# Optimization experiments

Measured on AMD Instinct MI355X. Metric: run time of the kernel, lower is better.

## Reference

```python
import jax, jax.numpy as jnp
import numpy as np

LAMBDA_ORD = 1.0
B, C = 65536, 256


def setup_inputs() -> dict:
    key = jax.random.key(0)
    k1, k2 = jax.random.split(key)
    predictions = jax.random.normal(k1, (B, C), dtype=jnp.float32)
    targets = jax.random.randint(k2, (B,), 0, C, dtype=jnp.int64)
    return {"predictions": predictions, "targets": targets}


def reference(predictions, targets):
    # Cross-entropy with mean reduction
    logp = jax.nn.log_softmax(predictions, axis=-1)          # [B, C]
    ce = -jnp.mean(jnp.take_along_axis(logp, targets[:, None], axis=1))
    # Ordinal penalty: mean_i sum_j softmax(pred_i)_j * (j - t_i)^2
    probs = jnp.exp(logp)                                     # [B, C]
    j = jnp.arange(predictions.shape[1], dtype=predictions.dtype)  # [C]
    dist2 = (j[None, :] - targets[:, None].astype(predictions.dtype)) ** 2  # [B, C]
    penalty = jnp.mean(jnp.sum(probs * dist2, axis=-1))
    return ce + LAMBDA_ORD * penalty
```

## Files before the change

kernel.cpp:

```cpp
#include <hip/hip_runtime.h>

#define NROWS  65536
#define NCLS   256
#define NBLK   2048
#define NLINE  64
#define BPL    (NBLK / NLINE)

struct __align__(128) Line { float v; int cnt; int pad[30]; };
__device__ Line g_line[NLINE];
__device__ int  g_master;

__global__ __launch_bounds__(256) void OrdinalLoss_main_kernel(
    const float* __restrict__ pred, const int* __restrict__ tgt,
    float* __restrict__ out, int nrows)
{
    const int tid    = blockIdx.x * blockDim.x + threadIdx.x;
    const int lane   = threadIdx.x & 63;
    const int g      = lane >> 4;
    const int li     = lane & 15;
    const int wave   = tid >> 6;
    const int nwaves = (gridDim.x * blockDim.x) >> 6;

    float acc = 0.0f;

    if (tid < nrows)
        acc = -pred[(size_t)tid * NCLS + tgt[tid]];

    const int npacks = nrows >> 2;
    for (int pack = wave; pack < npacks; pack += nwaves) {
        const int row = pack * 4 + g;
        const float* rp = pred + (size_t)row * NCLS + li * 4;

        const float4 p0 = *reinterpret_cast<const float4*>(rp);
        const float4 p1 = *reinterpret_cast<const float4*>(rp + 64);
        const float4 p2 = *reinterpret_cast<const float4*>(rp + 128);
        const float4 p3 = *reinterpret_cast<const float4*>(rp + 192);
        const float tf  = (float)tgt[row];
        const float j0  = (float)(li * 4);

        float s = 0.0f, w = 0.0f;
        #define TERM(pv, col) { float e = __expf(pv); s += e;              \
                                float d = (col) - tf; w = fmaf(e * d, d, w); }
        TERM(p0.x, j0 +   0.0f) TERM(p0.y, j0 +   1.0f)
        TERM(p0.z, j0 +   2.0f) TERM(p0.w, j0 +   3.0f)
        TERM(p1.x, j0 +  64.0f) TERM(p1.y, j0 +  65.0f)
        TERM(p1.z, j0 +  66.0f) TERM(p1.w, j0 +  67.0f)
        TERM(p2.x, j0 + 128.0f) TERM(p2.y, j0 + 129.0f)
        TERM(p2.z, j0 + 130.0f) TERM(p2.w, j0 + 131.0f)
        TERM(p3.x, j0 + 192.0f) TERM(p3.y, j0 + 193.0f)
        TERM(p3.z, j0 + 194.0f) TERM(p3.w, j0 + 195.0f)
        #undef TERM

        #pragma unroll
        for (int m = 8; m; m >>= 1) {
            s += __shfl_xor(s, m);
            w += __shfl_xor(w, m);
        }
        if (li == 0)
            acc += __logf(s) + w / s;
    }

    __shared__ float red[256];
    __shared__ int amLast;
    red[threadIdx.x] = acc;
    __syncthreads();
    float v = 0.0f;
    if (threadIdx.x < 64) {
        v = red[threadIdx.x] + red[threadIdx.x + 64] +
            red[threadIdx.x + 128] + red[threadIdx.x + 192];
        #pragma unroll
        for (int mask = 32; mask; mask >>= 1)
            v += __shfl_xor(v, mask);
    }

    if (threadIdx.x == 0) {
        amLast = 0;
        const int ln = blockIdx.x & (NLINE - 1);
        float old = atomicAdd(&g_line[ln].v, v * (1.0f / (float)NROWS));
        asm volatile("" :: "v"(old));
        if (atomicAdd(&g_line[ln].cnt, 1) == BPL - 1) {
            if (atomicAdd(&g_master, 1) == NLINE - 1)
                amLast = 1;
        }
    }
    __syncthreads();
    if (amLast) {
        if (threadIdx.x < NLINE) {
            float r = __hip_atomic_load(&g_line[threadIdx.x].v,
                                        __ATOMIC_RELAXED, __HIP_MEMORY_SCOPE_AGENT);
            #pragma unroll
            for (int mask = 32; mask; mask >>= 1)
                r += __shfl_xor(r, mask);
            if (threadIdx.x == 0)
                out[0] = r;
            __hip_atomic_store(&g_line[threadIdx.x].v, 0.0f,
                               __ATOMIC_RELAXED, __HIP_MEMORY_SCOPE_AGENT);
            __hip_atomic_store(&g_line[threadIdx.x].cnt, 0,
                               __ATOMIC_RELAXED, __HIP_MEMORY_SCOPE_AGENT);
            if (threadIdx.x == 0)
                __hip_atomic_store(&g_master, 0,
                                   __ATOMIC_RELAXED, __HIP_MEMORY_SCOPE_AGENT);
        }
    }
}

extern "C" void kernel_launch(void* const* d_in, const int* in_sizes, int n_in,
                              void* d_out, int out_size, void* d_ws, size_t ws_size,
                              hipStream_t stream) {
    const float* pred = (const float*)d_in[0];
    const int*   tgt  = (const int*)d_in[1];
    float*       out  = (float*)d_out;
    const int nrows   = in_sizes[1];

    OrdinalLoss_main_kernel<<<NBLK, 256, 0, stream>>>(pred, tgt, out, nrows);
}
```

Baseline: 19.71 us.

## Fuse target-logit gather into row pass, unroll two rows, use nontemporal loads

Removes the separate scattered gather of the target logit by picking it out of the already-loaded row registers and reducing it with the row sums. Expands the squared-distance term into three moment sums so the target value is only needed after the reduction. Processes two row packs per iteration with all eight vector loads issued up front to raise memory-level parallelism, and marks the loads nontemporal. This costs more shuffles and registers per row and adds select logic to extract the target value.

Measured after the change: 17.65 us. -10.5%, faster.

```diff
diff --git a/kernel.cpp b/kernel.cpp
--- a/kernel.cpp
+++ b/kernel.cpp
@@ -5,6 +5,8 @@
 #define NBLK   2048
 #define NLINE  64
 #define BPL    (NBLK / NLINE)
+
+typedef float nt_f4 __attribute__((ext_vector_type(4)));
 
 struct __align__(128) Line { float v; int cnt; int pad[30]; };
 __device__ Line g_line[NLINE];
@@ -22,43 +24,88 @@
     const int nwaves = (gridDim.x * blockDim.x) >> 6;
 
     float acc = 0.0f;
+    const float j0 = (float)(li * 4);
 
-    if (tid < nrows)
-        acc = -pred[(size_t)tid * NCLS + tgt[tid]];
+    #define TERM(S0, S1, S2, PV, OFF) {                                     \
+        const float d = j0 + (float)(OFF);                                  \
+        const float e = __expf(PV);                                         \
+        S0 += e;                                                            \
+        const float t1 = e * d;                                             \
+        S1 += t1;                                                           \
+        S2 = fmaf(t1, d, S2); }
+    #define PACK16(S0, S1, S2, Q0, Q1, Q2, Q3)                              \
+        TERM(S0,S1,S2, Q0[0],   0) TERM(S0,S1,S2, Q0[1],   1)               \
+        TERM(S0,S1,S2, Q0[2],   2) TERM(S0,S1,S2, Q0[3],   3)               \
+        TERM(S0,S1,S2, Q1[0],  64) TERM(S0,S1,S2, Q1[1],  65)               \
+        TERM(S0,S1,S2, Q1[2],  66) TERM(S0,S1,S2, Q1[3],  67)               \
+        TERM(S0,S1,S2, Q2[0], 128) TERM(S0,S1,S2, Q2[1], 129)               \
+        TERM(S0,S1,S2, Q2[2], 130) TERM(S0,S1,S2, Q2[3], 131)               \
+        TERM(S0,S1,S2, Q3[0], 192) TERM(S0,S1,S2, Q3[1], 193)               \
+        TERM(S0,S1,S2, Q3[2], 194) TERM(S0,S1,S2, Q3[3], 195)
+
+    #define PT(PTV, T, Q0, Q1, Q2, Q3) {                                    \
+        const int q = (T) >> 6, r = (T) & 3;                                \
+        const nt_f4 Q = (q==0) ? Q0 : (q==1) ? Q1 : (q==2) ? Q2 : Q3;       \
+        const float pv = (r==0) ? Q[0] : (r==1) ? Q[1] : (r==2) ? Q[2] : Q[3]; \
+        PTV = (li == (((T) >> 2) & 15)) ? pv : 0.0f; }
+
+    #define REDUCE4(S0, S1, S2, PTV, T)                                     \
+        _Pragma("unroll")                                                   \
+        for (int m = 8; m; m >>= 1) {                                       \
+            S0 += __shfl_xor(S0, m); S1 += __shfl_xor(S1, m);               \
+            S2 += __shfl_xor(S2, m); PTV += __shfl_xor(PTV, m);             \
+        }                                                                   \
+        if (li == 0) {                                                      \
+            const float tf = (float)(T);                                    \
+            acc += __logf(S0) - PTV                                         \
+                 + (S2 - 2.0f * tf * S1 + tf * tf * S0) / S0;               \
+        }
 
     const int npacks = nrows >> 2;
-    for (int pack = wave; pack < npacks; pack += nwaves) {
-        const int row = pack * 4 + g;
-        const float* rp = pred + (size_t)row * NCLS + li * 4;
+    int pack = wave;
+    for (; pack + nwaves < npacks; pack += 2 * nwaves) {
+        const int rowA = pack * 4 + g;
+        const int rowB = (pack + nwaves) * 4 + g;
+        const float* rpA = pred + (size_t)rowA * NCLS + li * 4;
+        const float* rpB = pred + (size_t)rowB * NCLS + li * 4;
+        const nt_f4 a0 = __builtin_nontemporal_load((const nt_f4*)(rpA));
+        const nt_f4 a1 = __builtin_nontemporal_load((const nt_f4*)(rpA + 64));
+        const nt_f4 a2 = __builtin_nontemporal_load((const nt_f4*)(rpA + 128));
+        const nt_f4 a3 = __builtin_nontemporal_load((const nt_f4*)(rpA + 192));
+        const nt_f4 b0 = __builtin_nontemporal_load((const nt_f4*)(rpB));
+        const nt_f4 b1 = __builtin_nontemporal_load((const nt_f4*)(rpB + 64));
+        const nt_f4 b2 = __builtin_nontemporal_load((const nt_f4*)(rpB + 128));
+        const nt_f4 b3 = __builtin_nontemporal_load((const nt_f4*)(rpB + 192));
+        const int tA = tgt[rowA];
+        const int tB = tgt[rowB];
 
-        const float4 p0 = *reinterpret_cast<const float4*>(rp);
-        const float4 p1 = *reinterpret_cast<const float4*>(rp + 64);
-        const float4 p2 = *reinterpret_cast<const float4*>(rp + 128);
-        const float4 p3 = *reinterpret_cast<const float4*>(rp + 192);
-        const float tf  = (float)tgt[row];
-        const float j0  = (float)(li * 4);
+        float sA0 = 0.0f, sA1 = 0.0f, sA2 = 0.0f, ptA;
+        PACK16(sA0, sA1, sA2, a0, a1, a2, a3)
+        PT(ptA, tA, a0, a1, a2, a3)
+        REDUCE4(sA0, sA1, sA2, ptA, tA)
 
-        float s = 0.0f, w = 0.0f;
-        #define TERM(pv, col) { float e = __expf(pv); s += e;              \
-                                float d = (col) - tf; w = fmaf(e * d, d, w); }
-        TERM(p0.x, j0 +   0.0f) TERM(p0.y, j0 +   1.0f)
-        TERM(p0.z, j0 +   2.0f) TERM(p0.w, j0 +   3.0f)
-        TERM(p1.x, j0 +  64.0f) TERM(p1.y, j0 +  65.0f)
-        TERM(p1.z, j0 +  66.0f) TERM(p1.w, j0 +  67.0f)
-        TERM(p2.x, j0 + 128.0f) TERM(p2.y, j0 + 129.0f)
-        TERM(p2.z, j0 + 130.0f) TERM(p2.w, j0 + 131.0f)
-        TERM(p3.x, j0 + 192.0f) TERM(p3.y, j0 + 193.0f)
-        TERM(p3.z, j0 + 194.0f) TERM(p3.w, j0 + 195.0f)
-        #undef TERM
-
-        #pragma unroll
-        for (int m = 8; m; m >>= 1) {
-            s += __shfl_xor(s, m);
-            w += __shfl_xor(w, m);
-        }
-        if (li == 0)
-            acc += __logf(s) + w / s;
+        float sB0 = 0.0f, sB1 = 0.0f, sB2 = 0.0f, ptB;
+        PACK16(sB0, sB1, sB2, b0, b1, b2, b3)
+        PT(ptB, tB, b0, b1, b2, b3)
+        REDUCE4(sB0, sB1, sB2, ptB, tB)
     }
+    if (pack < npacks) {
+        const int rowA = pack * 4 + g;
+        const float* rpA = pred + (size_t)rowA * NCLS + li * 4;
+        const nt_f4 a0 = __builtin_nontemporal_load((const nt_f4*)(rpA));
+        const nt_f4 a1 = __builtin_nontemporal_load((const nt_f4*)(rpA + 64));
+        const nt_f4 a2 = __builtin_nontemporal_load((const nt_f4*)(rpA + 128));
+        const nt_f4 a3 = __builtin_nontemporal_load((const nt_f4*)(rpA + 192));
+        const int tA = tgt[rowA];
+        float sA0 = 0.0f, sA1 = 0.0f, sA2 = 0.0f, ptA;
+        PACK16(sA0, sA1, sA2, a0, a1, a2, a3)
+        PT(ptA, tA, a0, a1, a2, a3)
+        REDUCE4(sA0, sA1, sA2, ptA, tA)
+    }
+    #undef TERM
+    #undef PACK16
+    #undef PT
+    #undef REDUCE4
 
     __shared__ float red[256];
     __shared__ int amLast;
```
